# Kernel optimization log

Hardware: AMD Instinct MI355X
Metric: run time of the kernel (lower is better)

## Reference

```python
import jax, jax.numpy as jnp
import numpy as np

B, N, CIN, CD, NE = 64, 256, 768, 32, 8192

def setup_inputs() -> dict:
    key = jax.random.key(0)
    ks = jax.random.split(key, 8)
    z = jax.random.normal(ks[0], (B, N, CIN), dtype=jnp.float32)
    # Embedding weight: trunc_normal_(mean=0, std=1, a=-3, b=3)
    emb_weight = jax.random.truncated_normal(ks[1], -3.0, 3.0, (NE, CD)).astype(jnp.float32)
    # Linears stored as [in, out] so y = x @ W + b
    W_compress = jax.random.normal(ks[2], (CIN, CD), dtype=jnp.float32) / np.sqrt(CIN)
    b_compress = jnp.zeros((CD,), dtype=jnp.float32)
    W_ct = jax.random.normal(ks[3], (CD, CD), dtype=jnp.float32) / np.sqrt(CD)
    b_ct = jnp.zeros((CD,), dtype=jnp.float32)
    W_expand = jax.random.normal(ks[4], (CD, CIN), dtype=jnp.float32) / np.sqrt(CD)
    b_expand = jnp.zeros((CIN,), dtype=jnp.float32)
    return {"z": z, "emb_weight": emb_weight, "W_compress": W_compress,
            "b_compress": b_compress, "W_ct": W_ct, "b_ct": b_ct,
            "W_expand": W_expand, "b_expand": b_expand}

def reference(z, emb_weight, W_compress, b_compress, W_ct, b_ct, W_expand, b_expand):
    sg = jax.lax.stop_gradient
    # torch uses embedding.weight.data -> detached codebook input
    implicit_codebook = sg(emb_weight) @ W_ct + b_ct              # [NE, CD]
    zc = z @ W_compress + b_compress                              # [B, N, CD]
    z_flat = zc.reshape(-1, zc.shape[-1])                         # [B*N, CD]
    # squared distance: ||z||^2 + ||c||^2 - 2 z.c
    d = (jnp.sum(z_flat ** 2, axis=1, keepdims=True)
         + jnp.sum(implicit_codebook ** 2, axis=1)
         - 2.0 * jnp.einsum('bd,nd->bn', z_flat, implicit_codebook))  # [B*N, NE]
    indices = jnp.argmin(d, axis=1)                               # [B*N]
    z_q = implicit_codebook[indices]                              # [B*N, CD]
    # training-path losses (codebook + 2.0 * commitment)
    loss = (jnp.mean((sg(z_q) - z_flat) ** 2)
            + 2.0 * jnp.mean((z_q - sg(z_flat)) ** 2))
    # straight-through estimator
    z_st = sg(z_q) + z_flat - sg(z_flat)
    out = z_st.reshape(zc.shape) @ W_expand + b_expand            # [B, N, CIN]
    return out, loss
```

## Files before the change

kernel.cpp:

```cpp
#include <hip/hip_runtime.h>

constexpr int CIN = 768;
constexpr int CD  = 32;
constexpr int NE  = 8192;
constexpr int M   = 16384;
constexpr int SCH = 64;
constexpr int CPC = NE / SCH;
constexpr int PTB = 256;
#define MARGIN 0.004f

typedef short short8 __attribute__((ext_vector_type(8)));
typedef float f32x4  __attribute__((ext_vector_type(4)));

__device__ inline void split_bf16(float x, unsigned short& h, unsigned short& l) {
  unsigned u = __float_as_uint(x);
  unsigned hb = (u + 0x7FFFu + ((u >> 16) & 1u)) >> 16;
  float hf = __uint_as_float(hb << 16);
  float r = x - hf;
  unsigned u2 = __float_as_uint(r);
  unsigned lb = (u2 + 0x7FFFu + ((u2 >> 16) & 1u)) >> 16;
  h = (unsigned short)hb;
  l = (unsigned short)lb;
}

__device__ inline void gload_lds16(const void* g, void* l) {
  __builtin_amdgcn_global_load_lds(
      (const __attribute__((address_space(1))) unsigned int*)g,
      (__attribute__((address_space(3))) unsigned int*)l, 16, 0, 0);
}

__global__ __launch_bounds__(256) void k_split(
    const float* __restrict__ Wc, const float* __restrict__ We,
    unsigned short* __restrict__ WcTh, unsigned short* __restrict__ WcTl,
    unsigned short* __restrict__ WeTh, unsigned short* __restrict__ WeTl) {
  const int t = threadIdx.x;
  if (blockIdx.x < 96) {
    const int idx = blockIdx.x * 256 + t;
    const int k = idx >> 5, n = idx & 31;
    unsigned short h, l;
    split_bf16(Wc[idx], h, l);
    WcTh[n * CIN + k] = h;
    WcTl[n * CIN + k] = l;
  } else {
    const int idx = (blockIdx.x - 96) * 256 + t;
    const int k = idx / CIN, n = idx - k * CIN;
    unsigned short h, l;
    split_bf16(We[idx], h, l);
    WeTh[n * CD + k] = h;
    WeTl[n * CD + k] = l;
  }
}

__global__ __launch_bounds__(256) void k_main(
    const float* __restrict__ z,
    const unsigned short* __restrict__ WcTh, const unsigned short* __restrict__ WcTl,
    const float* __restrict__ bc,
    const float* __restrict__ emb, const float* __restrict__ Wct,
    const float* __restrict__ bct,
    float* __restrict__ zc, unsigned short* __restrict__ zh,
    unsigned short* __restrict__ zl,
    float* __restrict__ cb, float* __restrict__ cbT, float* __restrict__ cnorm,
    unsigned short* __restrict__ ch, unsigned short* __restrict__ cl) {
  __shared__ float smem[1632];
  const int t = threadIdx.x;
  if (blockIdx.x >= 1024) {
    for (int i = t; i < CD * CD; i += 256) smem[i] = Wct[i];
    __syncthreads();
    const int g   = (blockIdx.x - 1024) * 256 + t;
    const int row = g >> 5;
    const int col = g & 31;
    float acc = bct[col];
    const float* er = emb + row * CD;
    #pragma unroll
    for (int k = 0; k < CD; ++k) acc = fmaf(er[k], smem[k * CD + col], acc);
    cb[g] = acc;
    cbT[(long)col * NE + row] = acc;
    unsigned short h, l;
    split_bf16(acc, h, l);
    ch[g] = h; cl[g] = l;
    float v = acc * acc;
    #pragma unroll
    for (int m = 16; m >= 1; m >>= 1) v += __shfl_xor(v, m, 64);
    if (col == 0) cnorm[row] = v;
    return;
  }
  float* ps = smem;
  const int lane = t & 63;
  const int wv   = t >> 6;
  const int n    = lane & 15;
  const int quad = lane >> 4;
  const int r0   = blockIdx.x * 16;

  const float* za = z + (long)(r0 + n) * CIN + wv * 192 + quad * 8;
  const unsigned short* bh0 = WcTh + n * CIN + wv * 192 + quad * 8;
  const unsigned short* bl0 = WcTl + n * CIN + wv * 192 + quad * 8;
  const unsigned short* bh1 = bh0 + 16 * CIN;
  const unsigned short* bl1 = bl0 + 16 * CIN;

  float4 zbuf[12];
  #pragma unroll
  for (int kt = 0; kt < 6; ++kt) {
    zbuf[2 * kt]     = *(const float4*)(za + kt * 32);
    zbuf[2 * kt + 1] = *(const float4*)(za + kt * 32 + 4);
  }

  f32x4 acc0, acc1;
  if (wv == 0) {
    const float b0 = bc[n];
    const float b1 = bc[n + 16];
    acc0 = (f32x4){b0, b0, b0, b0};
    acc1 = (f32x4){b1, b1, b1, b1};
  } else {
    acc0 = (f32x4){0.f, 0.f, 0.f, 0.f};
    acc1 = (f32x4){0.f, 0.f, 0.f, 0.f};
  }

  #pragma unroll
  for (int kt = 0; kt < 6; ++kt) {
    const float4 za0 = zbuf[2 * kt];
    const float4 za1 = zbuf[2 * kt + 1];
    short8 Ah, Al;
    {
      unsigned short h, l;
      split_bf16(za0.x, h, l); Ah[0] = (short)h; Al[0] = (short)l;
      split_bf16(za0.y, h, l); Ah[1] = (short)h; Al[1] = (short)l;
      split_bf16(za0.z, h, l); Ah[2] = (short)h; Al[2] = (short)l;
      split_bf16(za0.w, h, l); Ah[3] = (short)h; Al[3] = (short)l;
      split_bf16(za1.x, h, l); Ah[4] = (short)h; Al[4] = (short)l;
      split_bf16(za1.y, h, l); Ah[5] = (short)h; Al[5] = (short)l;
      split_bf16(za1.z, h, l); Ah[6] = (short)h; Al[6] = (short)l;
      split_bf16(za1.w, h, l); Ah[7] = (short)h; Al[7] = (short)l;
    }
    const short8 Bh0 = *(const short8*)(bh0 + kt * 32);
    const short8 Bl0 = *(const short8*)(bl0 + kt * 32);
    const short8 Bh1 = *(const short8*)(bh1 + kt * 32);
    const short8 Bl1 = *(const short8*)(bl1 + kt * 32);
    acc0 = __builtin_amdgcn_mfma_f32_16x16x32_bf16(Ah, Bh0, acc0, 0, 0, 0);
    acc0 = __builtin_amdgcn_mfma_f32_16x16x32_bf16(Ah, Bl0, acc0, 0, 0, 0);
    acc0 = __builtin_amdgcn_mfma_f32_16x16x32_bf16(Al, Bh0, acc0, 0, 0, 0);
    acc1 = __builtin_amdgcn_mfma_f32_16x16x32_bf16(Ah, Bh1, acc1, 0, 0, 0);
    acc1 = __builtin_amdgcn_mfma_f32_16x16x32_bf16(Ah, Bl1, acc1, 0, 0, 0);
    acc1 = __builtin_amdgcn_mfma_f32_16x16x32_bf16(Al, Bh1, acc1, 0, 0, 0);
  }

  if (wv != 0) {
    float* pp = ps + (wv - 1) * 544;
    #pragma unroll
    for (int r = 0; r < 4; ++r) {
      const int row = quad * 4 + r;
      pp[row * 17 + n]       = acc0[r];
      pp[272 + row * 17 + n] = acc1[r];
    }
  }
  __syncthreads();
  if (wv == 0) {
    #pragma unroll
    for (int r = 0; r < 4; ++r) {
      const int row = quad * 4 + r;
      const float v0 = ((acc0[r] + ps[row * 17 + n]) + ps[544 + row * 17 + n])
                       + ps[1088 + row * 17 + n];
      const float v1 = ((acc1[r] + ps[272 + row * 17 + n]) + ps[816 + row * 17 + n])
                       + ps[1360 + row * 17 + n];
      const long i0 = (long)(r0 + row) * CD + n;
      zc[i0]      = v0;
      zc[i0 + 16] = v1;
      unsigned short h, l;
      split_bf16(-2.f * v0, h, l); zh[i0] = h;      zl[i0] = l;
      split_bf16(-2.f * v1, h, l); zh[i0 + 16] = h; zl[i0 + 16] = l;
    }
  }
}

__global__ __launch_bounds__(256) void k_argmin(
    const unsigned short* __restrict__ zh, const unsigned short* __restrict__ zl,
    const unsigned short* __restrict__ ch, const unsigned short* __restrict__ cl,
    const float* __restrict__ cnorm,
    float* __restrict__ pd) {
  __shared__ __align__(16) unsigned short chs[2][CPC * CD];
  __shared__ __align__(16) unsigned short cls[2][CPC * CD];
  const int pb   = blockIdx.x & (M / PTB - 1);
  const int cp   = blockIdx.x >> 6;
  const int cid0 = cp * 2;
  const int lane = threadIdx.x & 63;
  const int wv   = threadIdx.x >> 6;
  const int col  = lane & 15;
  const int quad = lane >> 4;
  const int p0   = pb * PTB + wv * 64;

  const char* chg = (const char*)ch + (long)cid0 * (CPC * CD * 2);
  const char* clg = (const char*)cl + (long)cid0 * (CPC * CD * 2);
  #pragma unroll
  for (int s = 0; s < 4; ++s) {
    const int lo = s * 4096 + wv * 1024;
    gload_lds16(chg + lo + lane * 16, (char*)chs + lo);
    gload_lds16(clg + lo + lane * 16, (char*)cls + lo);
  }

  short8 Ah[4], Al[4];
  #pragma unroll
  for (int s = 0; s < 4; ++s) {
    Ah[s] = *(const short8*)(zh + (long)(p0 + s * 16 + col) * CD + quad * 8);
    Al[s] = *(const short8*)(zl + (long)(p0 + s * 16 + col) * CD + quad * 8);
  }

  float cnv[2][8];
  #pragma unroll
  for (int c2 = 0; c2 < 2; ++c2) {
    const int jb = (cid0 + c2) * CPC;
    #pragma unroll
    for (int tt = 0; tt < 8; ++tt) cnv[c2][tt] = cnorm[jb + tt * 16 + col];
  }

  __syncthreads();

  #pragma unroll
  for (int c2 = 0; c2 < 2; ++c2) {
    float bd[4][4];
    #pragma unroll
    for (int s = 0; s < 4; ++s)
      #pragma unroll
      for (int r = 0; r < 4; ++r) bd[s][r] = 1e30f;

    #pragma unroll
    for (int tt = 0; tt < 8; ++tt) {
      const short8 Bh = *(const short8*)(&chs[c2][(tt * 16 + col) * CD + quad * 8]);
      const short8 Bl = *(const short8*)(&cls[c2][(tt * 16 + col) * CD + quad * 8]);
      const f32x4 c4 = {cnv[c2][tt], cnv[c2][tt], cnv[c2][tt], cnv[c2][tt]};
      #pragma unroll
      for (int s = 0; s < 4; ++s) {
        f32x4 g = __builtin_amdgcn_mfma_f32_16x16x32_bf16(Ah[s], Bh, c4, 0, 0, 0);
        g = __builtin_amdgcn_mfma_f32_16x16x32_bf16(Ah[s], Bl, g, 0, 0, 0);
        g = __builtin_amdgcn_mfma_f32_16x16x32_bf16(Al[s], Bh, g, 0, 0, 0);
        #pragma unroll
        for (int r = 0; r < 4; ++r) bd[s][r] = fminf(bd[s][r], g[r]);
      }
    }

    #pragma unroll
    for (int mm = 1; mm <= 8; mm <<= 1) {
      #pragma unroll
      for (int s = 0; s < 4; ++s)
        #pragma unroll
        for (int r = 0; r < 4; ++r)
          bd[s][r] = fminf(bd[s][r], __shfl_xor(bd[s][r], mm, 64));
    }
    if (col == 0) {
      #pragma unroll
      for (int s = 0; s < 4; ++s)
        #pragma unroll
        for (int r = 0; r < 4; ++r) {
          const int pA = p0 + s * 16 + quad * 4 + r;
          pd[(long)pA * SCH + cid0 + c2] = bd[s][r];
        }
    }
  }
}

__global__ __launch_bounds__(256) void k_rescue(
    const float* __restrict__ zc, const float* __restrict__ cb,
    const float* __restrict__ cbT, const float* __restrict__ cnorm,
    const float* __restrict__ pd,
    float* __restrict__ zq, unsigned short* __restrict__ zqh,
    unsigned short* __restrict__ zql, float* __restrict__ lpart) {
  const int lane = threadIdx.x & 63;
  const int wv   = threadIdx.x >> 6;
  const int p    = blockIdx.x * 4 + wv;

  const float m = pd[(long)p * SCH + lane];
  float dstar = m;
  #pragma unroll
  for (int mm = 1; mm <= 32; mm <<= 1) dstar = fminf(dstar, __shfl_xor(dstar, mm, 64));
  unsigned long long mask = __ballot(m <= dstar + MARGIN);

  float zr[CD];
  {
    const float4* z4 = (const float4*)(zc + (long)p * CD);
    #pragma unroll
    for (int q = 0; q < 8; ++q) {
      float4 v = z4[q];
      zr[4 * q + 0] = v.x; zr[4 * q + 1] = v.y; zr[4 * q + 2] = v.z; zr[4 * q + 3] = v.w;
    }
  }

  float bd = 1e30f;
  int   bj = 0x7fffffff;
  while (mask) {
    const int c = (int)__builtin_ctzll(mask);
    mask &= mask - 1;
    const int j0 = c * CPC + 2 * lane;
    const float* cp = cbT + j0;
    float acc0 = 0.f, acc1 = 0.f;
    #pragma unroll
    for (int k = 0; k < CD; ++k) {
      const float2 cv = *(const float2*)(cp + (long)k * NE);
      acc0 = fmaf(zr[k], cv.x, acc0);
      acc1 = fmaf(zr[k], cv.y, acc1);
    }
    const float2 cn = *(const float2*)(cnorm + j0);
    const float d0 = fmaf(-2.f, acc0, cn.x);
    const float d1 = fmaf(-2.f, acc1, cn.y);
    if (d0 < bd) { bd = d0; bj = j0; }
    if (d1 < bd) { bd = d1; bj = j0 + 1; }
  }
  #pragma unroll
  for (int mm = 1; mm <= 32; mm <<= 1) {
    const float od = __shfl_xor(bd, mm, 64);
    const int   oj = __shfl_xor(bj, mm, 64);
    if (od < bd || (od == bd && oj < bj)) { bd = od; bj = oj; }
  }

  float ls = 0.f;
  if (lane < 32) {
    const float cv = cb[(long)bj * CD + lane];
    const float zv = zc[(long)p * CD + lane];
    zq[(long)p * CD + lane] = cv;
    unsigned short hh, ll;
    split_bf16(cv, hh, ll);
    zqh[(long)p * CD + lane] = hh;
    zql[(long)p * CD + lane] = ll;
    const float df = cv - zv;
    ls = df * df;
  }
  #pragma unroll
  for (int mm = 1; mm <= 32; mm <<= 1) ls += __shfl_xor(ls, mm, 64);
  if (lane == 0) lpart[p] = ls;
}

__global__ __launch_bounds__(256) void k_expand(
    const unsigned short* __restrict__ zqh, const unsigned short* __restrict__ zql,
    const unsigned short* __restrict__ WeTh, const unsigned short* __restrict__ WeTl,
    const float* __restrict__ be,
    const float* __restrict__ lpart,
    float* __restrict__ out,
    float* __restrict__ out_loss) {
  __shared__ float ob[16][260];
  __shared__ double redd[4];
  const int t = threadIdx.x;
  if (blockIdx.x == 3072) {
    double v = 0.0;
    for (int k = t; k < M; k += 256) v += (double)lpart[k];
    #pragma unroll
    for (int mm = 1; mm <= 32; mm <<= 1) v += __shfl_xor(v, mm, 64);
    if ((t & 63) == 0) redd[t >> 6] = v;
    __syncthreads();
    if (t == 0)
      out_loss[0] = (float)(3.0 * (redd[0] + redd[1] + redd[2] + redd[3]) / (double)(M * CD));
    return;
  }
  const int lane = t & 63;
  const int wv   = t >> 6;
  const int col  = lane & 15;
  const int quad = lane >> 4;
  const int rb   = blockIdx.x & 1023;
  const int cg   = blockIdx.x >> 10;
  const int r0   = rb * 16;

  const short8 Ah = *(const short8*)(zqh + (long)(r0 + col) * CD + quad * 8);
  const short8 Al = *(const short8*)(zql + (long)(r0 + col) * CD + quad * 8);

  #pragma unroll
  for (int tt = 0; tt < 4; ++tt) {
    const int n0 = cg * 256 + wv * 64 + tt * 16;
    const short8 Bh = *(const short8*)(WeTh + (long)(n0 + col) * CD + quad * 8);
    const short8 Bl = *(const short8*)(WeTl + (long)(n0 + col) * CD + quad * 8);
    const float bv = be[n0 + col];
    const f32x4 c4 = {bv, bv, bv, bv};
    f32x4 g = __builtin_amdgcn_mfma_f32_16x16x32_bf16(Ah, Bh, c4, 0, 0, 0);
    g = __builtin_amdgcn_mfma_f32_16x16x32_bf16(Ah, Bl, g, 0, 0, 0);
    g = __builtin_amdgcn_mfma_f32_16x16x32_bf16(Al, Bh, g, 0, 0, 0);
    #pragma unroll
    for (int r = 0; r < 4; ++r)
      ob[quad * 4 + r][wv * 64 + tt * 16 + col] = g[r];
  }
  __syncthreads();
  #pragma unroll
  for (int i = 0; i < 4; ++i) {
    const int f   = t + i * 256;
    const int row = f >> 6;
    const int c4  = f & 63;
    *(float4*)(out + (long)(r0 + row) * CIN + cg * 256 + c4 * 4) =
        *(const float4*)(&ob[row][c4 * 4]);
  }
}

extern "C" void kernel_launch(void* const* d_in, const int* in_sizes, int n_in,
                              void* d_out, int out_size, void* d_ws, size_t ws_size,
                              hipStream_t stream) {
  const float* z   = (const float*)d_in[0];
  const float* emb = (const float*)d_in[1];
  const float* Wc  = (const float*)d_in[2];
  const float* bc  = (const float*)d_in[3];
  const float* Wct = (const float*)d_in[4];
  const float* bct = (const float*)d_in[5];
  const float* We  = (const float*)d_in[6];
  const float* be  = (const float*)d_in[7];
  float* out = (float*)d_out;

  float* cb    = (float*)d_ws;
  float* cnorm = cb + NE * CD;
  float* zc    = cnorm + NE;
  float* zq    = zc + M * CD;
  float* pd    = zq + M * CD;
  float* lpart = pd + (long)M * SCH;
  unsigned short* zh   = (unsigned short*)(lpart + M);
  unsigned short* zl   = zh + M * CD;
  unsigned short* ch   = zl + M * CD;
  unsigned short* cl   = ch + NE * CD;
  unsigned short* zqh  = cl + NE * CD;
  unsigned short* zql  = zqh + M * CD;
  unsigned short* WeTh = zql + M * CD;
  unsigned short* WeTl = WeTh + CIN * CD;
  unsigned short* WcTh = WeTl + CIN * CD;
  unsigned short* WcTl = WcTh + CIN * CD;
  float* cbT = (float*)(WcTl + CIN * CD);

  k_split<<<192, 256, 0, stream>>>(Wc, We, WcTh, WcTl, WeTh, WeTl);
  k_main<<<2048, 256, 0, stream>>>(z, WcTh, WcTl, bc, emb, Wct, bct,
                                   zc, zh, zl, cb, cbT, cnorm, ch, cl);
  k_argmin<<<(M / PTB) * (SCH / 2), 256, 0, stream>>>(zh, zl, ch, cl, cnorm, pd);
  k_rescue<<<M / 4, 256, 0, stream>>>(zc, cb, cbT, cnorm, pd, zq, zqh, zql, lpart);
  k_expand<<<3072 + 1, 256, 0, stream>>>(zqh, zql, WeTh, WeTl, be, lpart,
                                         out, out + (long)M * CIN);
}
```

Before: 195.9 us.

## Fold weight split kernel into k_main and tile codebook transpose through LDS

Removes the separate k_split launch. k_main's compress blocks now read Wc directly and split it into bf16 hi/lo on the fly, while the codebook blocks also split and transpose W_expand. The cbT transpose write is staged through shared memory so global stores become contiguous runs of 8. This saves one launch and its serialization, but each compress block now does redundant strided fp32 loads of Wc plus split arithmetic.

```diff
diff --git a/kernel.cpp b/kernel.cpp
--- a/kernel.cpp
+++ b/kernel.cpp
@@ -29,44 +29,31 @@
       (__attribute__((address_space(3))) unsigned int*)l, 16, 0, 0);
 }
 
-__global__ __launch_bounds__(256) void k_split(
-    const float* __restrict__ Wc, const float* __restrict__ We,
-    unsigned short* __restrict__ WcTh, unsigned short* __restrict__ WcTl,
-    unsigned short* __restrict__ WeTh, unsigned short* __restrict__ WeTl) {
-  const int t = threadIdx.x;
-  if (blockIdx.x < 96) {
-    const int idx = blockIdx.x * 256 + t;
-    const int k = idx >> 5, n = idx & 31;
-    unsigned short h, l;
-    split_bf16(Wc[idx], h, l);
-    WcTh[n * CIN + k] = h;
-    WcTl[n * CIN + k] = l;
-  } else {
-    const int idx = (blockIdx.x - 96) * 256 + t;
-    const int k = idx / CIN, n = idx - k * CIN;
-    unsigned short h, l;
-    split_bf16(We[idx], h, l);
-    WeTh[n * CD + k] = h;
-    WeTl[n * CD + k] = l;
-  }
-}
-
 __global__ __launch_bounds__(256) void k_main(
-    const float* __restrict__ z,
-    const unsigned short* __restrict__ WcTh, const unsigned short* __restrict__ WcTl,
+    const float* __restrict__ z, const float* __restrict__ Wc,
     const float* __restrict__ bc,
     const float* __restrict__ emb, const float* __restrict__ Wct,
-    const float* __restrict__ bct,
+    const float* __restrict__ bct, const float* __restrict__ We,
     float* __restrict__ zc, unsigned short* __restrict__ zh,
     unsigned short* __restrict__ zl,
     float* __restrict__ cb, float* __restrict__ cbT, float* __restrict__ cnorm,
-    unsigned short* __restrict__ ch, unsigned short* __restrict__ cl) {
+    unsigned short* __restrict__ ch, unsigned short* __restrict__ cl,
+    unsigned short* __restrict__ WeTh, unsigned short* __restrict__ WeTl) {
   __shared__ float smem[1632];
   const int t = threadIdx.x;
   if (blockIdx.x >= 1024) {
+    const int bco = blockIdx.x - 1024;
+    if (t < 24) {
+      const int idx = bco * 24 + t;
+      const int k = idx / CIN, nn = idx - k * CIN;
+      unsigned short h, l;
+      split_bf16(We[idx], h, l);
+      WeTh[nn * CD + k] = h;
+      WeTl[nn * CD + k] = l;
+    }
     for (int i = t; i < CD * CD; i += 256) smem[i] = Wct[i];
     __syncthreads();
-    const int g   = (blockIdx.x - 1024) * 256 + t;
+    const int g   = bco * 256 + t;
     const int row = g >> 5;
     const int col = g & 31;
     float acc = bct[col];
@@ -74,7 +61,6 @@
     #pragma unroll
     for (int k = 0; k < CD; ++k) acc = fmaf(er[k], smem[k * CD + col], acc);
     cb[g] = acc;
-    cbT[(long)col * NE + row] = acc;
     unsigned short h, l;
     split_bf16(acc, h, l);
     ch[g] = h; cl[g] = l;
@@ -82,6 +68,13 @@
     #pragma unroll
     for (int m = 16; m >= 1; m >>= 1) v += __shfl_xor(v, m, 64);
     if (col == 0) cnorm[row] = v;
+    smem[1024 + col * 9 + (t >> 5)] = acc;
+    __syncthreads();
+    {
+      const int tc = t >> 3;
+      const int tr = t & 7;
+      cbT[(long)tc * NE + bco * 8 + tr] = smem[1024 + tc * 9 + tr];
+    }
     return;
   }
   float* ps = smem;
@@ -92,10 +85,6 @@
   const int r0   = blockIdx.x * 16;
 
   const float* za = z + (long)(r0 + n) * CIN + wv * 192 + quad * 8;
-  const unsigned short* bh0 = WcTh + n * CIN + wv * 192 + quad * 8;
-  const unsigned short* bl0 = WcTl + n * CIN + wv * 192 + quad * 8;
-  const unsigned short* bh1 = bh0 + 16 * CIN;
-  const unsigned short* bl1 = bl0 + 16 * CIN;
 
   float4 zbuf[12];
   #pragma unroll
@@ -131,10 +120,16 @@
       split_bf16(za1.z, h, l); Ah[6] = (short)h; Al[6] = (short)l;
       split_bf16(za1.w, h, l); Ah[7] = (short)h; Al[7] = (short)l;
     }
-    const short8 Bh0 = *(const short8*)(bh0 + kt * 32);
-    const short8 Bl0 = *(const short8*)(bl0 + kt * 32);
-    const short8 Bh1 = *(const short8*)(bh1 + kt * 32);
-    const short8 Bl1 = *(const short8*)(bl1 + kt * 32);
+    const int kb = wv * 192 + kt * 32 + quad * 8;
+    short8 Bh0, Bl0, Bh1, Bl1;
+    #pragma unroll
+    for (int j = 0; j < 8; ++j) {
+      unsigned short h, l;
+      split_bf16(Wc[(kb + j) * CD + n], h, l);
+      Bh0[j] = (short)h; Bl0[j] = (short)l;
+      split_bf16(Wc[(kb + j) * CD + n + 16], h, l);
+      Bh1[j] = (short)h; Bl1[j] = (short)l;
+    }
     acc0 = __builtin_amdgcn_mfma_f32_16x16x32_bf16(Ah, Bh0, acc0, 0, 0, 0);
     acc0 = __builtin_amdgcn_mfma_f32_16x16x32_bf16(Ah, Bl0, acc0, 0, 0, 0);
     acc0 = __builtin_amdgcn_mfma_f32_16x16x32_bf16(Al, Bh0, acc0, 0, 0, 0);
@@ -410,13 +405,10 @@
   unsigned short* zql  = zqh + M * CD;
   unsigned short* WeTh = zql + M * CD;
   unsigned short* WeTl = WeTh + CIN * CD;
-  unsigned short* WcTh = WeTl + CIN * CD;
-  unsigned short* WcTl = WcTh + CIN * CD;
-  float* cbT = (float*)(WcTl + CIN * CD);
-
-  k_split<<<192, 256, 0, stream>>>(Wc, We, WcTh, WcTl, WeTh, WeTl);
-  k_main<<<2048, 256, 0, stream>>>(z, WcTh, WcTl, bc, emb, Wct, bct,
-                                   zc, zh, zl, cb, cbT, cnorm, ch, cl);
+  float* cbT = (float*)(WeTl + CIN * CD);
+
+  k_main<<<2048, 256, 0, stream>>>(z, Wc, bc, emb, Wct, bct, We,
+                                   zc, zh, zl, cb, cbT, cnorm, ch, cl, WeTh, WeTl);
   k_argmin<<<(M / PTB) * (SCH / 2), 256, 0, stream>>>(zh, zl, ch, cl, cnorm, pd);
   k_rescue<<<M / 4, 256, 0, stream>>>(zc, cb, cbT, cnorm, pd, zq, zqh, zql, lpart);
   k_expand<<<3072 + 1, 256, 0, stream>>>(zqh, zql, WeTh, WeTl, be, lpart,
```

New measurement: 188.8 us, median of 2. -3.7%, faster.
